# Optimization experiments

Hardware: AMD Instinct MI355X
Metric: run time of the kernel (lower is better)

## Reference

```python
import jax, jax.numpy as jnp
import numpy as np

N = 1000000   # total nodes
F = 32        # node feature dim
E = 8         # edge feature dim
K = 16        # kernels per degree
COUNTS = [200000, 300000, 300000, 200000]  # focal nodes per degree 1..4
EPS = 1e-8


def _cos_mat(a, b):
    # a: [n, f], b: [k, f] -> cosine sim [n, k]
    num = a @ b.T
    den = jnp.linalg.norm(a, axis=-1)[:, None] * jnp.linalg.norm(b, axis=-1)[None, :]
    return num / jnp.maximum(den, EPS)


def _cos_pairs(a, b):
    # a: [n, d, f], b: [k, d, f] -> mean over d of per-slot cosine sim -> [n, k]
    num = jnp.einsum('ndf,kdf->nkd', a, b)
    den = jnp.linalg.norm(a, axis=-1)[:, None, :] * jnp.linalg.norm(b, axis=-1)[None, :, :]
    return jnp.mean(num / jnp.maximum(den, EPS), axis=-1)


def _deg_score(x, sel, nei, nei_p, nei_e, Wc, Wn, Wp, We, d):
    nd = sel.shape[0]
    x_focal = x[sel]                     # [nd, F] degree-grouped gather
    x_nei = x[nei].reshape(nd, d, F)     # [nd, d, F]
    sc = (_cos_mat(x_focal, Wc) + _cos_pairs(x_nei, Wn)
          + _cos_pairs(nei_p, Wp) + _cos_pairs(nei_e, We)) * 0.25
    return sc                            # [nd, K]


def setup_inputs() -> dict:
    key = jax.random.key(0)
    ks = iter(jax.random.split(key, 64))
    perm = jax.random.permutation(next(ks), N)  # degree buckets partition all nodes
    inp = {"x": jax.random.normal(next(ks), (N, F), jnp.float32)}
    off = 0
    for d in range(1, 5):
        nd = COUNTS[d - 1]
        inp[f"sel{d}"] = perm[off:off + nd]
        off += nd
        inp[f"nei{d}"] = jax.random.randint(next(ks), (nd * d,), 0, N)
        inp[f"nei_p{d}"] = jax.random.normal(next(ks), (nd, d, 3), jnp.float32)
        inp[f"nei_e{d}"] = jax.random.uniform(next(ks), (nd, d, E), jnp.float32)
        inp[f"Wc{d}"] = jax.random.normal(next(ks), (K, F), jnp.float32)
        inp[f"Wn{d}"] = jax.random.normal(next(ks), (K, d, F), jnp.float32)
        inp[f"Wp{d}"] = jax.random.normal(next(ks), (K, d, 3), jnp.float32)
        inp[f"We{d}"] = jax.random.normal(next(ks), (K, d, E), jnp.float32)
    return inp


def reference(x,
              sel1, nei1, nei_p1, nei_e1, Wc1, Wn1, Wp1, We1,
              sel2, nei2, nei_p2, nei_e2, Wc2, Wn2, Wp2, We2,
              sel3, nei3, nei_p3, nei_e3, Wc3, Wn3, Wp3, We3,
              sel4, nei4, nei_p4, nei_e4, Wc4, Wn4, Wp4, We4):
    groups = [
        (sel1, nei1, nei_p1, nei_e1, Wc1, Wn1, Wp1, We1),
        (sel2, nei2, nei_p2, nei_e2, Wc2, Wn2, Wp2, We2),
        (sel3, nei3, nei_p3, nei_e3, Wc3, Wn3, Wp3, We3),
        (sel4, nei4, nei_p4, nei_e4, Wc4, Wn4, Wp4, We4),
    ]
    # equivalent to: fill [sum_K, N] block matrix grouped by degree, reorder
    # columns by argsort of concatenated selected indices, then transpose.
    out = jnp.zeros((N, 4 * K), x.dtype)
    for i, (sel, nei, npos, ne, wc, wn, wp, we) in enumerate(groups):
        sc = _deg_score(x, sel, nei, npos, ne, wc, wn, wp, we, i + 1)
        out = out.at[sel, i * K:(i + 1) * K].set(sc)
    return out
```

## Files before the change

### kernel.cpp

```cpp
#include <hip/hip_runtime.h>
#include <stdint.h>

typedef _Float16 half8 __attribute__((ext_vector_type(8)));
typedef float floatx4 __attribute__((ext_vector_type(4)));
typedef float fvec4 __attribute__((ext_vector_type(4)));

struct WPtrs { const float *wc, *wn, *wp, *we; };

struct PrepArgs {
  const float* x; _Float16* xhat; int N; int nb_norm;
  const float* p[4]; const float* e[4]; _Float16* part[4];
  int nd[4];
  int pb[5];
  WPtrs w[4]; _Float16* psi;
};

template <int D>
__device__ inline void part_mfma(const PrepArgs& a, int g, int lblk, int tid,
                                 _Float16* lds) {
  constexpr int K16 = 16 * D;
  constexpr int K32 = ((D + 1) / 2) * 32;
  constexpr int NM  = K32 / 32;
  constexpr int RS  = K32 + 8;

  const float* __restrict__ p = a.p[g];
  const float* __restrict__ e = a.e[g];
  _Float16* __restrict__ part = a.part[g];
  int nd = a.nd[g];

  int lane = tid & 63, wv = tid >> 6;
  int r = lane & 15, c = lane >> 4;

  int node = lblk * 256 + tid;
  int nc = node < nd ? node : nd - 1;
  _Float16* arow = lds + (size_t)tid * RS;
#pragma unroll
  for (int s = 0; s < D; ++s) {
    const float* pp = p + ((size_t)nc * D + s) * 3;
    float a0 = pp[0], a1 = pp[1], a2 = pp[2];
    float n1 = sqrtf(a0 * a0 + a1 * a1 + a2 * a2);
    float r1 = n1 > 0.f ? 1.f / n1 : 0.f;
    const fvec4* ee = reinterpret_cast<const fvec4*>(e + ((size_t)nc * D + s) * 8);
    fvec4 e0 = ee[0], e1 = ee[1];
    float n2 = sqrtf(e0[0] * e0[0] + e0[1] * e0[1] + e0[2] * e0[2] + e0[3] * e0[3] +
                     e1[0] * e1[0] + e1[1] * e1[1] + e1[2] * e1[2] + e1[3] * e1[3]);
    float r2 = n2 > 0.f ? 1.f / n2 : 0.f;
    half8 h0, h1;
    h0[0] = (_Float16)(a0 * r1); h0[1] = (_Float16)(a1 * r1);
    h0[2] = (_Float16)(a2 * r1); h0[3] = (_Float16)0.f;
    h0[4] = (_Float16)(e0[0] * r2); h0[5] = (_Float16)(e0[1] * r2);
    h0[6] = (_Float16)(e0[2] * r2); h0[7] = (_Float16)(e0[3] * r2);
    h1[0] = (_Float16)(e1[0] * r2); h1[1] = (_Float16)(e1[1] * r2);
    h1[2] = (_Float16)(e1[2] * r2); h1[3] = (_Float16)(e1[3] * r2);
    h1[4] = (_Float16)0.f; h1[5] = (_Float16)0.f;
    h1[6] = (_Float16)0.f; h1[7] = (_Float16)0.f;
    *reinterpret_cast<half8*>(arow + s * 16)     = h0;
    *reinterpret_cast<half8*>(arow + s * 16 + 8) = h1;
  }
  if (K32 > K16) {
    half8 z = {};
    *reinterpret_cast<half8*>(arow + K16)     = z;
    *reinterpret_cast<half8*>(arow + K16 + 8) = z;
  }

  half8 bf[NM];
#pragma unroll
  for (int m = 0; m < NM; ++m) {
    int s = 2 * m + (c >> 1);
    if (s < D) {
      const float* sp = a.w[g].wp + ((size_t)r * D + s) * 3;
      float a0 = sp[0], a1 = sp[1], a2 = sp[2];
      float n1 = sqrtf(a0 * a0 + a1 * a1 + a2 * a2);
      float s1 = n1 > 0.f ? 0.25f / (D * n1) : 0.f;
      const float* se = a.w[g].we + ((size_t)r * D + s) * 8;
      float b0 = se[0], b1 = se[1], b2 = se[2], b3 = se[3];
      float b4 = se[4], b5 = se[5], b6 = se[6], b7 = se[7];
      float n2 = sqrtf(b0 * b0 + b1 * b1 + b2 * b2 + b3 * b3 +
                       b4 * b4 + b5 * b5 + b6 * b6 + b7 * b7);
      float s2 = n2 > 0.f ? 0.25f / (D * n2) : 0.f;
      half8 h;
      if ((c & 1) == 0) {
        h[0] = (_Float16)(a0 * s1); h[1] = (_Float16)(a1 * s1);
        h[2] = (_Float16)(a2 * s1); h[3] = (_Float16)0.f;
        h[4] = (_Float16)(b0 * s2); h[5] = (_Float16)(b1 * s2);
        h[6] = (_Float16)(b2 * s2); h[7] = (_Float16)(b3 * s2);
      } else {
        h[0] = (_Float16)(b4 * s2); h[1] = (_Float16)(b5 * s2);
        h[2] = (_Float16)(b6 * s2); h[3] = (_Float16)(b7 * s2);
        h[4] = (_Float16)0.f; h[5] = (_Float16)0.f;
        h[6] = (_Float16)0.f; h[7] = (_Float16)0.f;
      }
      bf[m] = h;
    } else {
      bf[m] = half8{};
    }
  }

  __builtin_amdgcn_wave_barrier();

#pragma unroll
  for (int q = 0; q < 4; ++q) {
    half8 af[NM];
#pragma unroll
    for (int m = 0; m < NM; ++m)
      af[m] = *reinterpret_cast<const half8*>(
          lds + (size_t)(wv * 64 + q * 16 + r) * RS + m * 32 + c * 8);
    floatx4 acc = {0.f, 0.f, 0.f, 0.f};
#pragma unroll
    for (int m = 0; m < NM; ++m)
      acc = __builtin_amdgcn_mfma_f32_16x16x32_f16(af[m], bf[m], acc, 0, 0, 0);
    int nb = lblk * 256 + wv * 64 + q * 16;
#pragma unroll
    for (int j = 0; j < 4; ++j) {
      int ng = nb + c * 4 + j;
      if (ng < nd) part[(size_t)ng * 16 + r] = (_Float16)acc[j];
    }
  }
}

__global__ __launch_bounds__(256) void k_prep(PrepArgs a) {
  __shared__ _Float16 lds[256 * 72];
  int bid = blockIdx.x, tid = threadIdx.x;

  if (bid < a.nb_norm) {
    int row = bid * 64 + (tid >> 2);
    int q   = tid & 3;
    if (row >= a.N) return;
    const fvec4* xr = reinterpret_cast<const fvec4*>(a.x + (size_t)row * 32 + q * 8);
    fvec4 va = xr[0], vb = xr[1];
    float ss = va[0] * va[0] + va[1] * va[1] + va[2] * va[2] + va[3] * va[3] +
               vb[0] * vb[0] + vb[1] * vb[1] + vb[2] * vb[2] + vb[3] * vb[3];
    ss += __shfl_xor(ss, 1);
    ss += __shfl_xor(ss, 2);
    float rn = ss > 0.f ? rsqrtf(ss) : 0.f;
    half8 h;
    h[0] = (_Float16)(va[0] * rn); h[1] = (_Float16)(va[1] * rn);
    h[2] = (_Float16)(va[2] * rn); h[3] = (_Float16)(va[3] * rn);
    h[4] = (_Float16)(vb[0] * rn); h[5] = (_Float16)(vb[1] * rn);
    h[6] = (_Float16)(vb[2] * rn); h[7] = (_Float16)(vb[3] * rn);
    *reinterpret_cast<half8*>(a.xhat + (size_t)row * 32 + q * 8) = h;
    return;
  }

  int b2 = bid - a.nb_norm;
  if (b2 < a.pb[4]) {
    if      (b2 < a.pb[1]) part_mfma<1>(a, 0, b2,           tid, lds);
    else if (b2 < a.pb[2]) part_mfma<2>(a, 1, b2 - a.pb[1], tid, lds);
    else if (b2 < a.pb[3]) part_mfma<3>(a, 2, b2 - a.pb[2], tid, lds);
    else                   part_mfma<4>(a, 3, b2 - a.pb[3], tid, lds);
    return;
  }

  int g = b2 - a.pb[4];
  int d = g + 1;
  int KD = 32 * (1 + d);
  _Float16* pg = a.psi + (size_t)g * (16 * 160);

  int k     = tid & 15;
  int piece = tid >> 4;
  if (piece > d) return;
  const float* src;
  float scale;
  if (piece == 0) { src = a.w[g].wc + k * 32;                           scale = 0.25f; }
  else            { src = a.w[g].wn + (size_t)(k * d + piece - 1) * 32; scale = 0.25f / d; }
  float ss = 0.f;
  for (int j = 0; j < 32; ++j) ss += src[j] * src[j];
  float n  = sqrtf(ss);
  float sc = n > 0.f ? scale / n : 0.f;
  _Float16* dst = pg + k * KD + 32 * piece;
  for (int j = 0; j < 32; ++j) dst[j] = (_Float16)(src[j] * sc);
}

struct MainArgs {
  const _Float16* xhat;
  const _Float16* part[4];
  const _Float16* psi;
  const int* sel[4];
  const int* nei[4];
  float* out;
  int nd[4];
  int blkOff[5];
};

template <int D, int NCH>
__device__ inline void main_one(const MainArgs& a, int g, int blk) {
  constexpr int NF = 1 + D;
  constexpr int KD = 32 * NF;

  const _Float16* xhat = a.xhat;
  const _Float16* part = a.part[g];
  const _Float16* psi  = a.psi + (size_t)g * (16 * 160);
  const int* sel = a.sel[g];
  const int* nei = a.nei[g];
  int nd = a.nd[g];

  int wave    = threadIdx.x >> 6;
  int lane    = threadIdx.x & 63;
  int nchunks = (nd + 15) >> 4;
  int chunk0  = (blk * 4 + wave) * NCH;
  if (chunk0 >= nchunks) return;
  int r = lane & 15;
  int c = lane >> 4;

  half8 bx[NF];
  {
    const _Float16* pb = psi + (size_t)r * KD + c * 8;
#pragma unroll
    for (int t = 0; t < NF; ++t)
      bx[t] = *reinterpret_cast<const half8*>(pb + 32 * t);
  }

  int riA[NCH];
  int sidx[NCH];
  int gidx[NCH][D];
#pragma unroll
  for (int u = 0; u < NCH; ++u) {
    int chunk = chunk0 + u;
    int ri = (chunk < nchunks) ? (chunk * 16 + r) : 0;
    if (ri > nd - 1) ri = nd - 1;
    riA[u]  = ri;
    sidx[u] = sel[ri];
  }
#pragma unroll
  for (int u = 0; u < NCH; ++u)
#pragma unroll
    for (int s = 0; s < D; ++s)
      gidx[u][s] = nei[(size_t)riA[u] * D + s];

  floatx4 acc[NCH];
#pragma unroll
  for (int u = 0; u < NCH; ++u) {
    int i0 = (chunk0 + u) << 4;
#pragma unroll
    for (int j = 0; j < 4; ++j) {
      int n = i0 + c * 4 + j;
      if (n > nd - 1) n = nd - 1;
      acc[u][j] = (float)part[(size_t)n * 16 + r];
    }
  }

  half8 af[NCH][NF];
#pragma unroll
  for (int u = 0; u < NCH; ++u) {
    af[u][0] = *reinterpret_cast<const half8*>(xhat + (size_t)sidx[u] * 32 + c * 8);
#pragma unroll
    for (int s = 0; s < D; ++s)
      af[u][1 + s] = *reinterpret_cast<const half8*>(xhat + (size_t)gidx[u][s] * 32 + c * 8);
  }

#pragma unroll
  for (int u = 0; u < NCH; ++u)
#pragma unroll
    for (int t = 0; t < NF; ++t)
      acc[u] = __builtin_amdgcn_mfma_f32_16x16x32_f16(af[u][t], bx[t], acc[u], 0, 0, 0);

#pragma unroll
  for (int u = 0; u < NCH; ++u) {
    int chunk = chunk0 + u;
    if (chunk >= nchunks) break;
    int i0 = chunk << 4;
#pragma unroll
    for (int j = 0; j < 4; ++j) {
      int n  = i0 + c * 4 + j;
      int so = __shfl(sidx[u], c * 4 + j);
      if (n < nd) {
        float* orow = a.out + (size_t)so * 64 + r;
#pragma unroll
        for (int q = 0; q < 4; ++q)
          orow[q * 16] = (q == D - 1) ? acc[u][j] : 0.f;
      }
    }
  }
}

__global__ __launch_bounds__(256) void k_main(MainArgs a) {
  int bid = blockIdx.x;
  if (bid < a.blkOff[1])      main_one<1, 6>(a, 0, bid);
  else if (bid < a.blkOff[2]) main_one<2, 5>(a, 1, bid - a.blkOff[1]);
  else if (bid < a.blkOff[3]) main_one<3, 4>(a, 2, bid - a.blkOff[2]);
  else                        main_one<4, 3>(a, 3, bid - a.blkOff[3]);
}

extern "C" void kernel_launch(void* const* d_in, const int* in_sizes, int n_in,
                              void* d_out, int out_size, void* d_ws, size_t ws_size,
                              hipStream_t stream) {
  const float* x = (const float*)d_in[0];
  int N = in_sizes[0] / 32;

  PrepArgs pa;
  MainArgs ma;
  pa.x = x; pa.N = N;
  int nd[4];
  for (int g = 0; g < 4; ++g) {
    int b = 1 + g * 8;
    ma.sel[g]  = (const int*)d_in[b + 0];
    ma.nei[g]  = (const int*)d_in[b + 1];
    pa.p[g]    = (const float*)d_in[b + 2];
    pa.e[g]    = (const float*)d_in[b + 3];
    pa.w[g].wc = (const float*)d_in[b + 4];
    pa.w[g].wn = (const float*)d_in[b + 5];
    pa.w[g].wp = (const float*)d_in[b + 6];
    pa.w[g].we = (const float*)d_in[b + 7];
    nd[g] = in_sizes[b];
    pa.nd[g] = nd[g];
    ma.nd[g] = nd[g];
  }
  ma.out = (float*)d_out;

  char* ws = (char*)d_ws;
  auto align256 = [](size_t o) { return (o + 255) & ~(size_t)255; };
  _Float16* xhat = (_Float16*)ws;
  size_t off = (size_t)N * 32 * 2;
  for (int g = 0; g < 4; ++g) {
    off = align256(off);
    pa.part[g] = (_Float16*)(ws + off);
    ma.part[g] = pa.part[g];
    off += (size_t)nd[g] * 16 * 2;
  }
  off = align256(off);
  _Float16* psi = (_Float16*)(ws + off);
  pa.psi = psi;
  ma.psi = psi;
  ma.xhat = xhat;
  pa.xhat = xhat;

  pa.nb_norm = (N + 63) / 64;
  pa.pb[0] = 0;
  for (int g = 0; g < 4; ++g) pa.pb[g + 1] = pa.pb[g] + (nd[g] + 255) / 256;
  int prep_blocks = pa.nb_norm + pa.pb[4] + 4;

  const int NCHg[4] = {6, 5, 4, 3};
  ma.blkOff[0] = 0;
  for (int g = 0; g < 4; ++g) {
    int ch = (nd[g] + 15) / 16;
    int perBlk = 4 * NCHg[g];
    ma.blkOff[g + 1] = ma.blkOff[g] + (ch + perBlk - 1) / perBlk;
  }

  k_prep<<<prep_blocks, 256, 0, stream>>>(pa);
  k_main<<<ma.blkOff[4], 256, 0, stream>>>(ma);
}
```

Baseline: 191.3 us.

## Fuse position/edge cosine partial scores into main gather kernel

Drops the prep-stage part_mfma pass that normalized nei_p/nei_e through LDS, ran an MFMA, and wrote fp16 partial scores to a workspace for the main kernel to read back. The main kernel now loads p and e per node, normalizes them in registers into MFMA A-fragments, and accumulates them with the Wp/We fragments before the feature MFMAs. This removes the partial-score write and read and shrinks the prep grid. In exchange the main kernel holds more registers per chunk and does the p/e loads and normalization itself, which may lower occupancy; each lane group also recomputes the norms for the slot it loads.

```diff
diff --git a/kernel.cpp b/kernel.cpp
--- a/kernel.cpp
+++ b/kernel.cpp
@@ -9,61 +9,95 @@
 
 struct PrepArgs {
   const float* x; _Float16* xhat; int N; int nb_norm;
-  const float* p[4]; const float* e[4]; _Float16* part[4];
-  int nd[4];
-  int pb[5];
   WPtrs w[4]; _Float16* psi;
 };
 
-template <int D>
-__device__ inline void part_mfma(const PrepArgs& a, int g, int lblk, int tid,
-                                 _Float16* lds) {
-  constexpr int K16 = 16 * D;
-  constexpr int K32 = ((D + 1) / 2) * 32;
-  constexpr int NM  = K32 / 32;
-  constexpr int RS  = K32 + 8;
-
-  const float* __restrict__ p = a.p[g];
-  const float* __restrict__ e = a.e[g];
-  _Float16* __restrict__ part = a.part[g];
+__global__ __launch_bounds__(256) void k_prep(PrepArgs a) {
+  int bid = blockIdx.x, tid = threadIdx.x;
+
+  if (bid < a.nb_norm) {
+    int row = bid * 64 + (tid >> 2);
+    int q   = tid & 3;
+    if (row >= a.N) return;
+    const fvec4* xr = reinterpret_cast<const fvec4*>(a.x + (size_t)row * 32 + q * 8);
+    fvec4 va = xr[0], vb = xr[1];
+    float ss = va[0] * va[0] + va[1] * va[1] + va[2] * va[2] + va[3] * va[3] +
+               vb[0] * vb[0] + vb[1] * vb[1] + vb[2] * vb[2] + vb[3] * vb[3];
+    ss += __shfl_xor(ss, 1);
+    ss += __shfl_xor(ss, 2);
+    float rn = ss > 0.f ? rsqrtf(ss) : 0.f;
+    half8 h;
+    h[0] = (_Float16)(va[0] * rn); h[1] = (_Float16)(va[1] * rn);
+    h[2] = (_Float16)(va[2] * rn); h[3] = (_Float16)(va[3] * rn);
+    h[4] = (_Float16)(vb[0] * rn); h[5] = (_Float16)(vb[1] * rn);
+    h[6] = (_Float16)(vb[2] * rn); h[7] = (_Float16)(vb[3] * rn);
+    *reinterpret_cast<half8*>(a.xhat + (size_t)row * 32 + q * 8) = h;
+    return;
+  }
+
+  int g = bid - a.nb_norm;
+  int d = g + 1;
+  int KD = 32 * (1 + d);
+  _Float16* pg = a.psi + (size_t)g * (16 * 160);
+
+  int k     = tid & 15;
+  int piece = tid >> 4;
+  if (piece > d) return;
+  const float* src;
+  float scale;
+  if (piece == 0) { src = a.w[g].wc + k * 32;                           scale = 0.25f; }
+  else            { src = a.w[g].wn + (size_t)(k * d + piece - 1) * 32; scale = 0.25f / d; }
+  float ss = 0.f;
+  for (int j = 0; j < 32; ++j) ss += src[j] * src[j];
+  float n  = sqrtf(ss);
+  float sc = n > 0.f ? scale / n : 0.f;
+  _Float16* dst = pg + k * KD + 32 * piece;
+  for (int j = 0; j < 32; ++j) dst[j] = (_Float16)(src[j] * sc);
+}
+
+struct MainArgs {
+  const _Float16* xhat;
+  const _Float16* psi;
+  const int* sel[4];
+  const int* nei[4];
+  const float* p[4];
+  const float* e[4];
+  WPtrs w[4];
+  float* out;
+  int nd[4];
+  int blkOff[5];
+};
+
+template <int D, int NCH>
+__device__ inline void main_one(const MainArgs& a, int g, int blk) {
+  constexpr int NF = 1 + D;
+  constexpr int KD = 32 * NF;
+  constexpr int NM = (D + 1) / 2;
+
+  const _Float16* xhat = a.xhat;
+  const _Float16* psi  = a.psi + (size_t)g * (16 * 160);
+  const int* sel = a.sel[g];
+  const int* nei = a.nei[g];
+  const float* __restrict__ pptr = a.p[g];
+  const float* __restrict__ eptr = a.e[g];
   int nd = a.nd[g];
 
-  int lane = tid & 63, wv = tid >> 6;
-  int r = lane & 15, c = lane >> 4;
-
-  int node = lblk * 256 + tid;
-  int nc = node < nd ? node : nd - 1;
-  _Float16* arow = lds + (size_t)tid * RS;
-#pragma unroll
-  for (int s = 0; s < D; ++s) {
-    const float* pp = p + ((size_t)nc * D + s) * 3;
-    float a0 = pp[0], a1 = pp[1], a2 = pp[2];
-    float n1 = sqrtf(a0 * a0 + a1 * a1 + a2 * a2);
-    float r1 = n1 > 0.f ? 1.f / n1 : 0.f;
-    const fvec4* ee = reinterpret_cast<const fvec4*>(e + ((size_t)nc * D + s) * 8);
-    fvec4 e0 = ee[0], e1 = ee[1];
-    float n2 = sqrtf(e0[0] * e0[0] + e0[1] * e0[1] + e0[2] * e0[2] + e0[3] * e0[3] +
-                     e1[0] * e1[0] + e1[1] * e1[1] + e1[2] * e1[2] + e1[3] * e1[3]);
-    float r2 = n2 > 0.f ? 1.f / n2 : 0.f;
-    half8 h0, h1;
-    h0[0] = (_Float16)(a0 * r1); h0[1] = (_Float16)(a1 * r1);
-    h0[2] = (_Float16)(a2 * r1); h0[3] = (_Float16)0.f;
-    h0[4] = (_Float16)(e0[0] * r2); h0[5] = (_Float16)(e0[1] * r2);
-    h0[6] = (_Float16)(e0[2] * r2); h0[7] = (_Float16)(e0[3] * r2);
-    h1[0] = (_Float16)(e1[0] * r2); h1[1] = (_Float16)(e1[1] * r2);
-    h1[2] = (_Float16)(e1[2] * r2); h1[3] = (_Float16)(e1[3] * r2);
-    h1[4] = (_Float16)0.f; h1[5] = (_Float16)0.f;
-    h1[6] = (_Float16)0.f; h1[7] = (_Float16)0.f;
-    *reinterpret_cast<half8*>(arow + s * 16)     = h0;
-    *reinterpret_cast<half8*>(arow + s * 16 + 8) = h1;
-  }
-  if (K32 > K16) {
-    half8 z = {};
-    *reinterpret_cast<half8*>(arow + K16)     = z;
-    *reinterpret_cast<half8*>(arow + K16 + 8) = z;
-  }
-
-  half8 bf[NM];
+  int wave    = threadIdx.x >> 6;
+  int lane    = threadIdx.x & 63;
+  int nchunks = (nd + 15) >> 4;
+  int chunk0  = (blk * 4 + wave) * NCH;
+  if (chunk0 >= nchunks) return;
+  int r = lane & 15;
+  int c = lane >> 4;
+
+  half8 bx[NF];
+  {
+    const _Float16* pb = psi + (size_t)r * KD + c * 8;
+#pragma unroll
+    for (int t = 0; t < NF; ++t)
+      bx[t] = *reinterpret_cast<const half8*>(pb + 32 * t);
+  }
+  half8 bpe[NM];
 #pragma unroll
   for (int m = 0; m < NM; ++m) {
     int s = 2 * m + (c >> 1);
@@ -90,124 +124,10 @@
         h[4] = (_Float16)0.f; h[5] = (_Float16)0.f;
         h[6] = (_Float16)0.f; h[7] = (_Float16)0.f;
       }
-      bf[m] = h;
+      bpe[m] = h;
     } else {
-      bf[m] = half8{};
+      bpe[m] = half8{};
     }
-  }
-
-  __builtin_amdgcn_wave_barrier();
-
-#pragma unroll
-  for (int q = 0; q < 4; ++q) {
-    half8 af[NM];
-#pragma unroll
-    for (int m = 0; m < NM; ++m)
-      af[m] = *reinterpret_cast<const half8*>(
-          lds + (size_t)(wv * 64 + q * 16 + r) * RS + m * 32 + c * 8);
-    floatx4 acc = {0.f, 0.f, 0.f, 0.f};
-#pragma unroll
-    for (int m = 0; m < NM; ++m)
-      acc = __builtin_amdgcn_mfma_f32_16x16x32_f16(af[m], bf[m], acc, 0, 0, 0);
-    int nb = lblk * 256 + wv * 64 + q * 16;
-#pragma unroll
-    for (int j = 0; j < 4; ++j) {
-      int ng = nb + c * 4 + j;
-      if (ng < nd) part[(size_t)ng * 16 + r] = (_Float16)acc[j];
-    }
-  }
-}
-
-__global__ __launch_bounds__(256) void k_prep(PrepArgs a) {
-  __shared__ _Float16 lds[256 * 72];
-  int bid = blockIdx.x, tid = threadIdx.x;
-
-  if (bid < a.nb_norm) {
-    int row = bid * 64 + (tid >> 2);
-    int q   = tid & 3;
-    if (row >= a.N) return;
-    const fvec4* xr = reinterpret_cast<const fvec4*>(a.x + (size_t)row * 32 + q * 8);
-    fvec4 va = xr[0], vb = xr[1];
-    float ss = va[0] * va[0] + va[1] * va[1] + va[2] * va[2] + va[3] * va[3] +
-               vb[0] * vb[0] + vb[1] * vb[1] + vb[2] * vb[2] + vb[3] * vb[3];
-    ss += __shfl_xor(ss, 1);
-    ss += __shfl_xor(ss, 2);
-    float rn = ss > 0.f ? rsqrtf(ss) : 0.f;
-    half8 h;
-    h[0] = (_Float16)(va[0] * rn); h[1] = (_Float16)(va[1] * rn);
-    h[2] = (_Float16)(va[2] * rn); h[3] = (_Float16)(va[3] * rn);
-    h[4] = (_Float16)(vb[0] * rn); h[5] = (_Float16)(vb[1] * rn);
-    h[6] = (_Float16)(vb[2] * rn); h[7] = (_Float16)(vb[3] * rn);
-    *reinterpret_cast<half8*>(a.xhat + (size_t)row * 32 + q * 8) = h;
-    return;
-  }
-
-  int b2 = bid - a.nb_norm;
-  if (b2 < a.pb[4]) {
-    if      (b2 < a.pb[1]) part_mfma<1>(a, 0, b2,           tid, lds);
-    else if (b2 < a.pb[2]) part_mfma<2>(a, 1, b2 - a.pb[1], tid, lds);
-    else if (b2 < a.pb[3]) part_mfma<3>(a, 2, b2 - a.pb[2], tid, lds);
-    else                   part_mfma<4>(a, 3, b2 - a.pb[3], tid, lds);
-    return;
-  }
-
-  int g = b2 - a.pb[4];
-  int d = g + 1;
-  int KD = 32 * (1 + d);
-  _Float16* pg = a.psi + (size_t)g * (16 * 160);
-
-  int k     = tid & 15;
-  int piece = tid >> 4;
-  if (piece > d) return;
-  const float* src;
-  float scale;
-  if (piece == 0) { src = a.w[g].wc + k * 32;                           scale = 0.25f; }
-  else            { src = a.w[g].wn + (size_t)(k * d + piece - 1) * 32; scale = 0.25f / d; }
-  float ss = 0.f;
-  for (int j = 0; j < 32; ++j) ss += src[j] * src[j];
-  float n  = sqrtf(ss);
-  float sc = n > 0.f ? scale / n : 0.f;
-  _Float16* dst = pg + k * KD + 32 * piece;
-  for (int j = 0; j < 32; ++j) dst[j] = (_Float16)(src[j] * sc);
-}
-
-struct MainArgs {
-  const _Float16* xhat;
-  const _Float16* part[4];
-  const _Float16* psi;
-  const int* sel[4];
-  const int* nei[4];
-  float* out;
-  int nd[4];
-  int blkOff[5];
-};
-
-template <int D, int NCH>
-__device__ inline void main_one(const MainArgs& a, int g, int blk) {
-  constexpr int NF = 1 + D;
-  constexpr int KD = 32 * NF;
-
-  const _Float16* xhat = a.xhat;
-  const _Float16* part = a.part[g];
-  const _Float16* psi  = a.psi + (size_t)g * (16 * 160);
-  const int* sel = a.sel[g];
-  const int* nei = a.nei[g];
-  int nd = a.nd[g];
-
-  int wave    = threadIdx.x >> 6;
-  int lane    = threadIdx.x & 63;
-  int nchunks = (nd + 15) >> 4;
-  int chunk0  = (blk * 4 + wave) * NCH;
-  if (chunk0 >= nchunks) return;
-  int r = lane & 15;
-  int c = lane >> 4;
-
-  half8 bx[NF];
-  {
-    const _Float16* pb = psi + (size_t)r * KD + c * 8;
-#pragma unroll
-    for (int t = 0; t < NF; ++t)
-      bx[t] = *reinterpret_cast<const half8*>(pb + 32 * t);
   }
 
   int riA[NCH];
@@ -227,18 +147,6 @@
     for (int s = 0; s < D; ++s)
       gidx[u][s] = nei[(size_t)riA[u] * D + s];
 
-  floatx4 acc[NCH];
-#pragma unroll
-  for (int u = 0; u < NCH; ++u) {
-    int i0 = (chunk0 + u) << 4;
-#pragma unroll
-    for (int j = 0; j < 4; ++j) {
-      int n = i0 + c * 4 + j;
-      if (n > nd - 1) n = nd - 1;
-      acc[u][j] = (float)part[(size_t)n * 16 + r];
-    }
-  }
-
   half8 af[NCH][NF];
 #pragma unroll
   for (int u = 0; u < NCH; ++u) {
@@ -248,11 +156,52 @@
       af[u][1 + s] = *reinterpret_cast<const half8*>(xhat + (size_t)gidx[u][s] * 32 + c * 8);
   }
 
-#pragma unroll
-  for (int u = 0; u < NCH; ++u)
+  half8 ap[NCH][NM];
+#pragma unroll
+  for (int u = 0; u < NCH; ++u) {
+#pragma unroll
+    for (int m = 0; m < NM; ++m) {
+      int s = 2 * m + (c >> 1);
+      if (s < D) {
+        const float* pp = pptr + ((size_t)riA[u] * D + s) * 3;
+        float a0 = pp[0], a1 = pp[1], a2 = pp[2];
+        float n1 = sqrtf(a0 * a0 + a1 * a1 + a2 * a2);
+        float r1 = n1 > 0.f ? 1.f / n1 : 0.f;
+        const fvec4* ee = reinterpret_cast<const fvec4*>(eptr + ((size_t)riA[u] * D + s) * 8);
+        fvec4 e0 = ee[0], e1 = ee[1];
+        float n2 = sqrtf(e0[0] * e0[0] + e0[1] * e0[1] + e0[2] * e0[2] + e0[3] * e0[3] +
+                         e1[0] * e1[0] + e1[1] * e1[1] + e1[2] * e1[2] + e1[3] * e1[3]);
+        float r2 = n2 > 0.f ? 1.f / n2 : 0.f;
+        half8 h;
+        if ((c & 1) == 0) {
+          h[0] = (_Float16)(a0 * r1);   h[1] = (_Float16)(a1 * r1);
+          h[2] = (_Float16)(a2 * r1);   h[3] = (_Float16)0.f;
+          h[4] = (_Float16)(e0[0] * r2); h[5] = (_Float16)(e0[1] * r2);
+          h[6] = (_Float16)(e0[2] * r2); h[7] = (_Float16)(e0[3] * r2);
+        } else {
+          h[0] = (_Float16)(e1[0] * r2); h[1] = (_Float16)(e1[1] * r2);
+          h[2] = (_Float16)(e1[2] * r2); h[3] = (_Float16)(e1[3] * r2);
+          h[4] = (_Float16)0.f; h[5] = (_Float16)0.f;
+          h[6] = (_Float16)0.f; h[7] = (_Float16)0.f;
+        }
+        ap[u][m] = h;
+      } else {
+        ap[u][m] = half8{};
+      }
+    }
+  }
+
+  floatx4 acc[NCH];
+#pragma unroll
+  for (int u = 0; u < NCH; ++u) {
+    acc[u] = floatx4{0.f, 0.f, 0.f, 0.f};
+#pragma unroll
+    for (int m = 0; m < NM; ++m)
+      acc[u] = __builtin_amdgcn_mfma_f32_16x16x32_f16(ap[u][m], bpe[m], acc[u], 0, 0, 0);
 #pragma unroll
     for (int t = 0; t < NF; ++t)
       acc[u] = __builtin_amdgcn_mfma_f32_16x16x32_f16(af[u][t], bx[t], acc[u], 0, 0, 0);
+  }
 
 #pragma unroll
   for (int u = 0; u < NCH; ++u) {
@@ -295,14 +244,14 @@
     int b = 1 + g * 8;
     ma.sel[g]  = (const int*)d_in[b + 0];
     ma.nei[g]  = (const int*)d_in[b + 1];
-    pa.p[g]    = (const float*)d_in[b + 2];
-    pa.e[g]    = (const float*)d_in[b + 3];
+    ma.p[g]    = (const float*)d_in[b + 2];
+    ma.e[g]    = (const float*)d_in[b + 3];
     pa.w[g].wc = (const float*)d_in[b + 4];
     pa.w[g].wn = (const float*)d_in[b + 5];
     pa.w[g].wp = (const float*)d_in[b + 6];
     pa.w[g].we = (const float*)d_in[b + 7];
+    ma.w[g]    = pa.w[g];
     nd[g] = in_sizes[b];
-    pa.nd[g] = nd[g];
     ma.nd[g] = nd[g];
   }
   ma.out = (float*)d_out;
@@ -310,24 +259,15 @@
   char* ws = (char*)d_ws;
   auto align256 = [](size_t o) { return (o + 255) & ~(size_t)255; };
   _Float16* xhat = (_Float16*)ws;
-  size_t off = (size_t)N * 32 * 2;
-  for (int g = 0; g < 4; ++g) {
-    off = align256(off);
-    pa.part[g] = (_Float16*)(ws + off);
-    ma.part[g] = pa.part[g];
-    off += (size_t)nd[g] * 16 * 2;
-  }
-  off = align256(off);
+  size_t off = align256((size_t)N * 32 * 2);
   _Float16* psi = (_Float16*)(ws + off);
-  pa.psi = psi;
-  ma.psi = psi;
+  pa.xhat = xhat;
+  pa.psi  = psi;
   ma.xhat = xhat;
-  pa.xhat = xhat;
+  ma.psi  = psi;
 
   pa.nb_norm = (N + 63) / 64;
-  pa.pb[0] = 0;
-  for (int g = 0; g < 4; ++g) pa.pb[g + 1] = pa.pb[g] + (nd[g] + 255) / 256;
-  int prep_blocks = pa.nb_norm + pa.pb[4] + 4;
+  int prep_blocks = pa.nb_norm + 4;
 
   const int NCHg[4] = {6, 5, 4, 3};
   ma.blkOff[0] = 0;
```

Result: slower. 206.6 us (+8.0%).
